# Kernel tuning notes

Hardware: AMD Instinct MI355X
Metric: run time of the kernel (lower is better)

## Reference

```python
import jax, jax.numpy as jnp
import numpy as np

D_MODEL = 1024
NUM_HEADS = 16
D_HEAD = D_MODEL // NUM_HEADS
THETA = 10000.0


def setup_inputs() -> dict:
    key = jax.random.key(0)
    ks = jax.random.split(key, 5)
    B, S = 2, 2048
    std = np.sqrt(2.0 / (D_MODEL + D_MODEL))
    return {
        "x": jax.random.normal(ks[0], (B, S, D_MODEL), dtype=jnp.float32),
        "token_positions": jnp.arange(S, dtype=jnp.int32),
        "wq": jax.random.normal(ks[1], (D_MODEL, D_MODEL), dtype=jnp.float32) * std,
        "wk": jax.random.normal(ks[2], (D_MODEL, D_MODEL), dtype=jnp.float32) * std,
        "wv": jax.random.normal(ks[3], (D_MODEL, D_MODEL), dtype=jnp.float32) * std,
        "wo": jax.random.normal(ks[4], (D_MODEL, D_MODEL), dtype=jnp.float32) * std,
    }


def _rope(x, token_positions):
    # x: [B, H, S, D_HEAD]; token_positions: [S]
    freq_idx = jnp.arange(0, D_HEAD, 2, dtype=jnp.float32)
    inv_freq = THETA ** (-freq_idx / D_HEAD)                      # [D_HEAD/2]
    angles = token_positions.astype(jnp.float32)[:, None] * inv_freq  # [S, D_HEAD/2]
    cos = jnp.cos(angles)[None, None, :, :]
    sin = jnp.sin(angles)[None, None, :, :]
    x_even = x[..., 0::2]
    x_odd = x[..., 1::2]
    rot_even = x_even * cos - x_odd * sin
    rot_odd = x_even * sin + x_odd * cos
    # interleave pairs back: [..., pairs, 2] -> [..., D_HEAD]
    return jnp.stack((rot_even, rot_odd), axis=-1).reshape(x.shape)


def reference(x, token_positions, wq, wk, wv, wo):
    B, S, _ = x.shape
    def proj(w):
        y = jnp.einsum('bsi,oi->bso', x, w)
        return y.reshape(B, S, NUM_HEADS, D_HEAD).transpose(0, 2, 1, 3)  # [B,H,S,Dh]
    q = _rope(proj(wq), token_positions)
    k = _rope(proj(wk), token_positions)
    v = proj(wv)
    scores = jnp.einsum('bhqd,bhkd->bhqk', q, k) / jnp.sqrt(jnp.float32(D_HEAD))
    causal = jnp.tril(jnp.ones((S, S), dtype=bool))
    scores = jnp.where(causal, scores, -jnp.inf)
    probs = jax.nn.softmax(scores, axis=-1)
    attn = jnp.einsum('bhqk,bhkd->bhqd', probs, v)
    attn = attn.transpose(0, 2, 1, 3).reshape(B, S, D_MODEL)
    return jnp.einsum('bsi,oi->bso', attn, wo)
```

## Files before the change

kernel.cpp:

```cpp
#include <hip/hip_runtime.h>
#include <math.h>

#define D_MODEL 1024
#define NUM_HEADS 16
#define D_HEAD 64
#define SEQ 2048
#define BATCH 2

typedef __attribute__((ext_vector_type(8))) short short8;
typedef __attribute__((ext_vector_type(4))) short short4v;
typedef __attribute__((ext_vector_type(4))) float float4v;

__device__ __forceinline__ short f2bf(float f) {
    unsigned u = __float_as_uint(f);
    u += 0x7FFFu + ((u >> 16) & 1u);
    return (short)(u >> 16);
}

__global__ __launch_bounds__(256) void cvt_bf16_kernel(
    const float* __restrict__ x,  const float* __restrict__ wq,
    const float* __restrict__ wk, const float* __restrict__ wv,
    const float* __restrict__ wo, const int* __restrict__ pos,
    short* __restrict__ xb,  short* __restrict__ wqb,
    short* __restrict__ wkb, short* __restrict__ wvb,
    short* __restrict__ wob,
    float* __restrict__ costab, float* __restrict__ sintab)
{
    const int a = blockIdx.y;
    if (a == 5) {
        const int idx = blockIdx.x * 256 + threadIdx.x;
        if (idx < SEQ * 32) {
            const int s = idx >> 5, fi = idx & 31;
            const float p = (float)pos[s];
            const float inv_freq = exp2f((float)fi * -0.4152410118609203f);
            float sn, cs;
            sincosf(p * inv_freq, &sn, &cs);
            costab[idx] = cs;
            sintab[idx] = sn;
        }
        return;
    }
    const float* src = (a == 0) ? x : (a == 1) ? wq : (a == 2) ? wk : (a == 3) ? wv : wo;
    short* dst = (a == 0) ? xb : (a == 1) ? wqb : (a == 2) ? wkb : (a == 3) ? wvb : wob;
    const int n = (a == 0) ? (BATCH * SEQ * D_MODEL) : (D_MODEL * D_MODEL);
    const int i = (blockIdx.x * 256 + threadIdx.x) * 8;
    if (i >= n) return;
    const float4 v0 = *(const float4*)(src + i);
    const float4 v1 = *(const float4*)(src + i + 4);
    short8 r;
    r[0] = f2bf(v0.x); r[1] = f2bf(v0.y); r[2] = f2bf(v0.z); r[3] = f2bf(v0.w);
    r[4] = f2bf(v1.x); r[5] = f2bf(v1.y); r[6] = f2bf(v1.z); r[7] = f2bf(v1.w);
    *(short8*)(dst + i) = r;
}

__device__ __forceinline__ void gemm_core_db(
    const short* __restrict__ a, const short* __restrict__ b,
    short* smem, int m0, int n0, float4v acc[4][4])
{
    const int tid = threadIdx.x;
    const int lane = tid & 63;
    const int l15 = lane & 15, quad = lane >> 4;
    const int wave = tid >> 6;
    const int mw = (wave & 1) * 64, nw = (wave >> 1) * 64;
    const int srow = tid >> 2;
    const int scol = (tid & 3) * 8;

    const short* ag = a + (size_t)(m0 + srow) * D_MODEL + scol;
    const short* bg = b + (size_t)(n0 + srow) * D_MODEL + scol;

    short* bufA[2] = { smem,        smem + 8192 };
    short* bufB[2] = { smem + 4096, smem + 12288 };

    short8 ga0 = *(const short8*)(ag);
    short8 ga1 = *(const short8*)(ag + (size_t)64 * D_MODEL);
    short8 gb0 = *(const short8*)(bg);
    short8 gb1 = *(const short8*)(bg + (size_t)64 * D_MODEL);
    *(short8*)&bufA[0][srow * 32 + scol]        = ga0;
    *(short8*)&bufA[0][(64 + srow) * 32 + scol] = ga1;
    *(short8*)&bufB[0][srow * 32 + scol]        = gb0;
    *(short8*)&bufB[0][(64 + srow) * 32 + scol] = gb1;
    ga0 = *(const short8*)(ag + 32);
    ga1 = *(const short8*)(ag + 32 + (size_t)64 * D_MODEL);
    gb0 = *(const short8*)(bg + 32);
    gb1 = *(const short8*)(bg + 32 + (size_t)64 * D_MODEL);

    for (int k = 0; k < 32; k++) {
        __syncthreads();
        if (k + 1 < 32) {
            short* bA = bufA[(k + 1) & 1];
            short* bB = bufB[(k + 1) & 1];
            *(short8*)&bA[srow * 32 + scol]        = ga0;
            *(short8*)&bA[(64 + srow) * 32 + scol] = ga1;
            *(short8*)&bB[srow * 32 + scol]        = gb0;
            *(short8*)&bB[(64 + srow) * 32 + scol] = gb1;
        }
        if (k + 2 < 32) {
            const int off = (k + 2) * 32;
            ga0 = *(const short8*)(ag + off);
            ga1 = *(const short8*)(ag + off + (size_t)64 * D_MODEL);
            gb0 = *(const short8*)(bg + off);
            gb1 = *(const short8*)(bg + off + (size_t)64 * D_MODEL);
        }
        const short* lA = bufA[k & 1];
        const short* lB = bufB[k & 1];
        short8 af[4], bf[4];
        #pragma unroll
        for (int i = 0; i < 4; i++)
            af[i] = *(const short8*)&lA[(mw + i * 16 + l15) * 32 + quad * 8];
        #pragma unroll
        for (int i = 0; i < 4; i++)
            bf[i] = *(const short8*)&lB[(nw + i * 16 + l15) * 32 + quad * 8];
        #pragma unroll
        for (int mi = 0; mi < 4; mi++)
            #pragma unroll
            for (int ni = 0; ni < 4; ni++)
                acc[mi][ni] = __builtin_amdgcn_mfma_f32_16x16x32_bf16(
                    af[mi], bf[ni], acc[mi][ni], 0, 0, 0);
    }
}

__global__ __launch_bounds__(256) void qkv_mfma_kernel(
    const short* __restrict__ xb, const short* __restrict__ wqb,
    const short* __restrict__ wkb, const short* __restrict__ wvb,
    const float* __restrict__ costab, const float* __restrict__ sintab,
    short* __restrict__ Qb, short* __restrict__ Kb, short* __restrict__ Vt)
{
    __shared__ __align__(16) short smem[128 * 136];

    const int z = blockIdx.x >> 8;
    const int bid = blockIdx.x & 255;
    const int m0 = (bid & 31) * 128;
    const int n0 = (bid >> 5) * 128;
    const short* w = (z == 0) ? wqb : (z == 1) ? wkb : wvb;

    float4v acc[4][4];
    #pragma unroll
    for (int i = 0; i < 4; i++)
        #pragma unroll
        for (int j = 0; j < 4; j++)
            acc[i][j] = (float4v){0.f, 0.f, 0.f, 0.f};

    gemm_core_db(xb, w, smem, m0, n0, acc);

    const int tid = threadIdx.x;
    const int lane = tid & 63;
    const int l15 = lane & 15, quad = lane >> 4;
    const int wave = tid >> 6;
    const int mw = (wave & 1) * 64, nw = (wave >> 1) * 64;
    const int s_base = m0 & (SEQ - 1);
    const int bb = m0 >> 11;

    __syncthreads();

    if (z == 2) {
        #pragma unroll
        for (int ni = 0; ni < 4; ni++) {
            #pragma unroll
            for (int mi = 0; mi < 4; mi++) {
                #pragma unroll
                for (int r = 0; r < 4; r++)
                    smem[(nw + ni * 16 + l15) * 136 + mw + mi * 16 + quad * 4 + r] =
                        f2bf(acc[mi][ni][r]);
            }
        }
        __syncthreads();
        #pragma unroll
        for (int it = 0; it < 8; it++) {
            const int nloc = it * 16 + (tid >> 4);
            const int mloc = (tid & 15) * 8;
            const short8 val = *(const short8*)&smem[nloc * 136 + mloc];
            const int n = n0 + nloc;
            const int h = n >> 6, d = n & 63;
            *(short8*)(Vt + ((size_t)(bb * NUM_HEADS + h) * D_HEAD + d) * SEQ +
                       s_base + mloc) = val;
        }
    } else {
        short* dst = (z == 0) ? Qb : Kb;
        const float qs = (z == 0) ? 0.125f : 1.0f;
        #pragma unroll
        for (int ni = 0; ni < 4; ni++) {
            const int n = n0 + nw + ni * 16 + l15;
            const int d = n & 63;
            const int fi = d >> 1;
            #pragma unroll
            for (int mi = 0; mi < 4; mi++) {
                #pragma unroll
                for (int r = 0; r < 4; r++) {
                    const int mloc = mw + mi * 16 + quad * 4 + r;
                    const int ti = ((s_base + mloc) << 5) + fi;
                    const float cs = costab[ti];
                    const float sn = sintab[ti];
                    const float val = acc[mi][ni][r];
                    const float partner = __shfl_xor(val, 1, 64);
                    const float res = (l15 & 1) ? fmaf(partner, sn, val * cs)
                                                : fmaf(val, cs, -partner * sn);
                    smem[mloc * 136 + nw + ni * 16 + l15] = f2bf(res * qs);
                }
            }
        }
        __syncthreads();
        #pragma unroll
        for (int it = 0; it < 8; it++) {
            const int ri = it * 32 + (tid >> 3);
            const int mloc = ri & 127;
            const int hh = ri >> 7;
            const int nloc = hh * 64 + (tid & 7) * 8;
            const short8 val = *(const short8*)&smem[mloc * 136 + nloc];
            const int n = n0 + nloc;
            const int h = n >> 6, d = n & 63;
            *(short8*)(dst + ((size_t)(bb * NUM_HEADS + h) * SEQ + s_base + mloc) *
                       D_HEAD + d) = val;
        }
    }
}

__global__ __launch_bounds__(256) void attn_mfma_kernel(
    const short* __restrict__ Qb, const short* __restrict__ Kb,
    const short* __restrict__ Vt, short* __restrict__ Ab)
{
    __shared__ __align__(16) short lK[64 * 72];
    __shared__ __align__(16) short lV[64 * 72];
    __shared__ __align__(16) short lP[4][16 * 72];

    const int tid = threadIdx.x;
    const int lane = tid & 63;
    const int wave = tid >> 6;
    const int l15 = lane & 15;
    const int quad = lane >> 4;

    const int bh = blockIdx.x & (BATCH * NUM_HEADS - 1);
    const int qt = (SEQ / 64 - 1) - (blockIdx.x >> 5);
    const int q0w = qt * 64 + wave * 16;
    const int qcmp = q0w + l15;

    const short* Kg = Kb + (size_t)bh * SEQ * D_HEAD;
    const short* Vg = Vt + (size_t)bh * D_HEAD * SEQ;

    const short* Qrow = Qb + ((size_t)bh * SEQ + q0w + l15) * D_HEAD;
    const short8 qf0 = *(const short8*)(Qrow + quad * 8);
    const short8 qf1 = *(const short8*)(Qrow + 32 + quad * 8);

    float4v o0 = {0.f, 0.f, 0.f, 0.f}, o1 = o0, o2 = o0, o3 = o0;
    float lp = 0.f;

    const int nt = qt + 1;
    const int srow = tid >> 2;
    const int sch = (tid & 3) * 8;

    short8 k0 = *(const short8*)(Kg + (size_t)srow * D_HEAD + sch);
    short8 k1 = *(const short8*)(Kg + (size_t)srow * D_HEAD + sch + 32);
    short8 v0 = *(const short8*)(Vg + (size_t)srow * SEQ + sch);
    short8 v1 = *(const short8*)(Vg + (size_t)srow * SEQ + sch + 32);

    for (int t = 0; t < nt; t++) {
        const int kt0 = t * 64;
        __syncthreads();
        *(short8*)&lK[srow * 72 + sch]      = k0;
        *(short8*)&lK[srow * 72 + sch + 32] = k1;
        *(short8*)&lV[srow * 72 + sch]      = v0;
        *(short8*)&lV[srow * 72 + sch + 32] = v1;
        __syncthreads();
        if (t + 1 < nt) {
            k0 = *(const short8*)(Kg + (size_t)(kt0 + 64 + srow) * D_HEAD + sch);
            k1 = *(const short8*)(Kg + (size_t)(kt0 + 64 + srow) * D_HEAD + sch + 32);
            v0 = *(const short8*)(Vg + (size_t)srow * SEQ + kt0 + 64 + sch);
            v1 = *(const short8*)(Vg + (size_t)srow * SEQ + kt0 + 64 + sch + 32);
        }

        short* Pw = lP[wave];
        #pragma unroll
        for (int g = 0; g < 4; g++) {
            float4v s = {0.f, 0.f, 0.f, 0.f};
            const short8 ka = *(const short8*)&lK[(g * 16 + l15) * 72 + quad * 8];
            s = __builtin_amdgcn_mfma_f32_16x16x32_bf16(ka, qf0, s, 0, 0, 0);
            const short8 kb = *(const short8*)&lK[(g * 16 + l15) * 72 + 32 + quad * 8];
            s = __builtin_amdgcn_mfma_f32_16x16x32_bf16(kb, qf1, s, 0, 0, 0);

            const int kbase = kt0 + g * 16 + quad * 4;
            short4v pk;
            #pragma unroll
            for (int r = 0; r < 4; r++) {
                const float e = (kbase + r <= qcmp) ? __expf(s[r]) : 0.f;
                lp += e;
                pk[r] = f2bf(e);
            }
            *(short4v*)&Pw[l15 * 72 + g * 16 + quad * 4] = pk;
        }

        const short8 pa0 = *(const short8*)&lP[wave][l15 * 72 + quad * 8];
        const short8 pa1 = *(const short8*)&lP[wave][l15 * 72 + 32 + quad * 8];

        {
            const short8 va = *(const short8*)&lV[(0 * 16 + l15) * 72 + quad * 8];
            const short8 vb = *(const short8*)&lV[(0 * 16 + l15) * 72 + 32 + quad * 8];
            o0 = __builtin_amdgcn_mfma_f32_16x16x32_bf16(pa0, va, o0, 0, 0, 0);
            o0 = __builtin_amdgcn_mfma_f32_16x16x32_bf16(pa1, vb, o0, 0, 0, 0);
        }
        {
            const short8 va = *(const short8*)&lV[(1 * 16 + l15) * 72 + quad * 8];
            const short8 vb = *(const short8*)&lV[(1 * 16 + l15) * 72 + 32 + quad * 8];
            o1 = __builtin_amdgcn_mfma_f32_16x16x32_bf16(pa0, va, o1, 0, 0, 0);
            o1 = __builtin_amdgcn_mfma_f32_16x16x32_bf16(pa1, vb, o1, 0, 0, 0);
        }
        {
            const short8 va = *(const short8*)&lV[(2 * 16 + l15) * 72 + quad * 8];
            const short8 vb = *(const short8*)&lV[(2 * 16 + l15) * 72 + 32 + quad * 8];
            o2 = __builtin_amdgcn_mfma_f32_16x16x32_bf16(pa0, va, o2, 0, 0, 0);
            o2 = __builtin_amdgcn_mfma_f32_16x16x32_bf16(pa1, vb, o2, 0, 0, 0);
        }
        {
            const short8 va = *(const short8*)&lV[(3 * 16 + l15) * 72 + quad * 8];
            const short8 vb = *(const short8*)&lV[(3 * 16 + l15) * 72 + 32 + quad * 8];
            o3 = __builtin_amdgcn_mfma_f32_16x16x32_bf16(pa0, va, o3, 0, 0, 0);
            o3 = __builtin_amdgcn_mfma_f32_16x16x32_bf16(pa1, vb, o3, 0, 0, 0);
        }
    }

    lp += __shfl_xor(lp, 16, 64);
    lp += __shfl_xor(lp, 32, 64);

    const int b = bh >> 4, h = bh & 15;
    short* Ap = Ab + ((size_t)(b * SEQ) + q0w + quad * 4) * D_MODEL + h * D_HEAD;
    #pragma unroll
    for (int r = 0; r < 4; r++) {
        const float inv = 1.0f / __shfl(lp, quad * 4 + r, 64);
        Ap[(size_t)r * D_MODEL + l15]      = f2bf(o0[r] * inv);
        Ap[(size_t)r * D_MODEL + 16 + l15] = f2bf(o1[r] * inv);
        Ap[(size_t)r * D_MODEL + 32 + l15] = f2bf(o2[r] * inv);
        Ap[(size_t)r * D_MODEL + 48 + l15] = f2bf(o3[r] * inv);
    }
}

__global__ __launch_bounds__(256) void out_mfma_kernel(
    const short* __restrict__ Ab, const short* __restrict__ wob,
    float* __restrict__ out)
{
    __shared__ __align__(16) short smem[2 * 8192];

    const int bid = blockIdx.x;
    const int m0 = (bid & 31) * 128;
    const int n0 = (bid >> 5) * 128;

    float4v acc[4][4];
    #pragma unroll
    for (int i = 0; i < 4; i++)
        #pragma unroll
        for (int j = 0; j < 4; j++)
            acc[i][j] = (float4v){0.f, 0.f, 0.f, 0.f};

    gemm_core_db(Ab, wob, smem, m0, n0, acc);

    const int tid = threadIdx.x;
    const int lane = tid & 63;
    const int l15 = lane & 15, quad = lane >> 4;
    const int wave = tid >> 6;
    const int mw = (wave & 1) * 64, nw = (wave >> 1) * 64;

    #pragma unroll
    for (int mi = 0; mi < 4; mi++) {
        #pragma unroll
        for (int r = 0; r < 4; r++) {
            const int m = m0 + mw + mi * 16 + quad * 4 + r;
            float* op = out + (size_t)m * D_MODEL + n0 + nw + l15;
            #pragma unroll
            for (int ni = 0; ni < 4; ni++)
                op[ni * 16] = acc[mi][ni][r];
        }
    }
}

extern "C" void kernel_launch(void* const* d_in, const int* in_sizes, int n_in,
                              void* d_out, int out_size, void* d_ws, size_t ws_size,
                              hipStream_t stream)
{
    const float* x  = (const float*)d_in[0];
    const int*  pos = (const int*)d_in[1];
    const float* wq = (const float*)d_in[2];
    const float* wk = (const float*)d_in[3];
    const float* wv = (const float*)d_in[4];
    const float* wo = (const float*)d_in[5];
    float* out = (float*)d_out;

    const size_t nx = (size_t)BATCH * SEQ * D_MODEL;
    const size_t nw = (size_t)D_MODEL * D_MODEL;
    short* xb  = (short*)d_ws;
    short* wqb = xb + nx;
    short* wkb = wqb + nw;
    short* wvb = wkb + nw;
    short* wob = wvb + nw;
    short* Qb  = wob + nw;
    short* Kb  = Qb + nx;
    short* Vt  = Kb + nx;
    short* Ab  = Vt + nx;
    float* costab = (float*)(Ab + nx);
    float* sintab = costab + SEQ * 32;

    dim3 blk(256);
    cvt_bf16_kernel<<<dim3(2048, 6), blk, 0, stream>>>(x, wq, wk, wv, wo, pos,
                                                       xb, wqb, wkb, wvb, wob,
                                                       costab, sintab);
    qkv_mfma_kernel<<<dim3(768), blk, 0, stream>>>(xb, wqb, wkb, wvb,
                                                   costab, sintab, Qb, Kb, Vt);
    attn_mfma_kernel<<<dim3(BATCH * NUM_HEADS * (SEQ / 64)), blk, 0, stream>>>(Qb, Kb, Vt, Ab);
    out_mfma_kernel<<<dim3(256), blk, 0, stream>>>(Ab, wob, out);
}
```

Baseline: 187.8 us.

## Load GEMM tiles directly into LDS with global_load_lds, single-buffered

Replaces the register-staged, double-buffered GEMM tile loads with direct global-to-LDS loads (global_load_lds, 16 bytes per lane), and shrinks the out-projection shared-memory buffer to one stage. This removes the VGPR round-trip and the separate LDS store instructions and may improve occupancy through lower LDS and register use. In exchange it drops the prefetch overlap: each k-step now issues its loads and waits on a barrier before computing, so load latency is exposed unless other resident blocks hide it.

```diff
diff --git a/kernel.cpp b/kernel.cpp
--- a/kernel.cpp
+++ b/kernel.cpp
@@ -16,6 +16,11 @@
     u += 0x7FFFu + ((u >> 16) & 1u);
     return (short)(u >> 16);
 }
+
+#define GLOAD_LDS16(g, l)                                                     \
+    __builtin_amdgcn_global_load_lds(                                         \
+        (const __attribute__((address_space(1))) unsigned int*)(g),           \
+        (__attribute__((address_space(3))) unsigned int*)(l), 16, 0, 0)
 
 __global__ __launch_bounds__(256) void cvt_bf16_kernel(
     const float* __restrict__ x,  const float* __restrict__ wq,
@@ -53,9 +58,9 @@
     *(short8*)(dst + i) = r;
 }
 
-__device__ __forceinline__ void gemm_core_db(
+__device__ __forceinline__ void gemm_core_lds(
     const short* __restrict__ a, const short* __restrict__ b,
-    short* smem, int m0, int n0, float4v acc[4][4])
+    short* lA, short* lB, int m0, int n0, float4v acc[4][4])
 {
     const int tid = threadIdx.x;
     const int lane = tid & 63;
@@ -67,42 +72,17 @@
 
     const short* ag = a + (size_t)(m0 + srow) * D_MODEL + scol;
     const short* bg = b + (size_t)(n0 + srow) * D_MODEL + scol;
-
-    short* bufA[2] = { smem,        smem + 8192 };
-    short* bufB[2] = { smem + 4096, smem + 12288 };
-
-    short8 ga0 = *(const short8*)(ag);
-    short8 ga1 = *(const short8*)(ag + (size_t)64 * D_MODEL);
-    short8 gb0 = *(const short8*)(bg);
-    short8 gb1 = *(const short8*)(bg + (size_t)64 * D_MODEL);
-    *(short8*)&bufA[0][srow * 32 + scol]        = ga0;
-    *(short8*)&bufA[0][(64 + srow) * 32 + scol] = ga1;
-    *(short8*)&bufB[0][srow * 32 + scol]        = gb0;
-    *(short8*)&bufB[0][(64 + srow) * 32 + scol] = gb1;
-    ga0 = *(const short8*)(ag + 32);
-    ga1 = *(const short8*)(ag + 32 + (size_t)64 * D_MODEL);
-    gb0 = *(const short8*)(bg + 32);
-    gb1 = *(const short8*)(bg + 32 + (size_t)64 * D_MODEL);
-
-    for (int k = 0; k < 32; k++) {
-        __syncthreads();
-        if (k + 1 < 32) {
-            short* bA = bufA[(k + 1) & 1];
-            short* bB = bufB[(k + 1) & 1];
-            *(short8*)&bA[srow * 32 + scol]        = ga0;
-            *(short8*)&bA[(64 + srow) * 32 + scol] = ga1;
-            *(short8*)&bB[srow * 32 + scol]        = gb0;
-            *(short8*)&bB[(64 + srow) * 32 + scol] = gb1;
-        }
-        if (k + 2 < 32) {
-            const int off = (k + 2) * 32;
-            ga0 = *(const short8*)(ag + off);
-            ga1 = *(const short8*)(ag + off + (size_t)64 * D_MODEL);
-            gb0 = *(const short8*)(bg + off);
-            gb1 = *(const short8*)(bg + off + (size_t)64 * D_MODEL);
-        }
-        const short* lA = bufA[k & 1];
-        const short* lB = bufB[k & 1];
+    short* lAd = lA + tid * 8;
+    short* lBd = lB + tid * 8;
+
+    for (int k0 = 0; k0 < D_MODEL; k0 += 32) {
+        __syncthreads();
+        GLOAD_LDS16(ag + k0, lAd);
+        GLOAD_LDS16(ag + k0 + (size_t)64 * D_MODEL, lAd + 2048);
+        GLOAD_LDS16(bg + k0, lBd);
+        GLOAD_LDS16(bg + k0 + (size_t)64 * D_MODEL, lBd + 2048);
+        __syncthreads();
+
         short8 af[4], bf[4];
         #pragma unroll
         for (int i = 0; i < 4; i++)
@@ -140,7 +120,7 @@
         for (int j = 0; j < 4; j++)
             acc[i][j] = (float4v){0.f, 0.f, 0.f, 0.f};
 
-    gemm_core_db(xb, w, smem, m0, n0, acc);
+    gemm_core_lds(xb, w, smem, smem + 4096, m0, n0, acc);
 
     const int tid = threadIdx.x;
     const int lane = tid & 63;
@@ -335,7 +315,7 @@
     const short* __restrict__ Ab, const short* __restrict__ wob,
     float* __restrict__ out)
 {
-    __shared__ __align__(16) short smem[2 * 8192];
+    __shared__ __align__(16) short smem[8192];
 
     const int bid = blockIdx.x;
     const int m0 = (bid & 31) * 128;
@@ -348,7 +328,7 @@
         for (int j = 0; j < 4; j++)
             acc[i][j] = (float4v){0.f, 0.f, 0.f, 0.f};
 
-    gemm_core_db(Ab, wob, smem, m0, n0, acc);
+    gemm_core_lds(Ab, wob, smem, smem + 4096, m0, n0, acc);
 
     const int tid = threadIdx.x;
     const int lane = tid & 63;
```

Measured after the change: 214.1 us. 14.0% more time.

## Process two 64-row query tiles per attention block to reuse K/V loads

Applied to the files above, without the earlier changes.

Each attention workgroup now handles 128 query rows, with every wave owning two 16-row query groups (A and B), so each K/V tile staged in LDS is reused by twice as many queries. The grid is halved and the upper group's extra causal tile runs only the B path through a per-wave activity check. This cuts global K/V traffic and barrier count per query. The cost is more registers and LDS per block, fewer blocks for the causal load-balance, and some wave divergence on the last tile.

```diff
diff --git a/kernel.cpp b/kernel.cpp
--- a/kernel.cpp
+++ b/kernel.cpp
@@ -220,7 +220,8 @@
 {
     __shared__ __align__(16) short lK[64 * 72];
     __shared__ __align__(16) short lV[64 * 72];
-    __shared__ __align__(16) short lP[4][16 * 72];
+    __shared__ __align__(16) short lPA[4][16 * 72];
+    __shared__ __align__(16) short lPB[4][16 * 72];
 
     const int tid = threadIdx.x;
     const int lane = tid & 63;
@@ -229,21 +230,28 @@
     const int quad = lane >> 4;
 
     const int bh = blockIdx.x & (BATCH * NUM_HEADS - 1);
-    const int qt = (SEQ / 64 - 1) - (blockIdx.x >> 5);
-    const int q0w = qt * 64 + wave * 16;
-    const int qcmp = q0w + l15;
+    const int qt = (SEQ / 128 - 1) - (blockIdx.x >> 5);
+    const int q0b = qt * 128;
+    const int qA = q0b + wave * 16;
+    const int qB = qA + 64;
+    const int qcA = qA + l15;
+    const int qcB = qB + l15;
 
     const short* Kg = Kb + (size_t)bh * SEQ * D_HEAD;
     const short* Vg = Vt + (size_t)bh * D_HEAD * SEQ;
 
-    const short* Qrow = Qb + ((size_t)bh * SEQ + q0w + l15) * D_HEAD;
-    const short8 qf0 = *(const short8*)(Qrow + quad * 8);
-    const short8 qf1 = *(const short8*)(Qrow + 32 + quad * 8);
-
-    float4v o0 = {0.f, 0.f, 0.f, 0.f}, o1 = o0, o2 = o0, o3 = o0;
-    float lp = 0.f;
-
-    const int nt = qt + 1;
+    const short* QrowA = Qb + ((size_t)bh * SEQ + qA + l15) * D_HEAD;
+    const short8 qa0 = *(const short8*)(QrowA + quad * 8);
+    const short8 qa1 = *(const short8*)(QrowA + 32 + quad * 8);
+    const short* QrowB = Qb + ((size_t)bh * SEQ + qB + l15) * D_HEAD;
+    const short8 qb0 = *(const short8*)(QrowB + quad * 8);
+    const short8 qb1 = *(const short8*)(QrowB + 32 + quad * 8);
+
+    float4v oA0 = {0.f,0.f,0.f,0.f}, oA1 = oA0, oA2 = oA0, oA3 = oA0;
+    float4v oB0 = oA0, oB1 = oA0, oB2 = oA0, oB3 = oA0;
+    float lpA = 0.f, lpB = 0.f;
+
+    const int nt = (qt + 1) * 2;
     const int srow = tid >> 2;
     const int sch = (tid & 3) * 8;
 
@@ -267,67 +275,90 @@
             v1 = *(const short8*)(Vg + (size_t)srow * SEQ + kt0 + 64 + sch + 32);
         }
 
-        short* Pw = lP[wave];
+        const bool actA = (kt0 <= qA + 15);
+
         #pragma unroll
         for (int g = 0; g < 4; g++) {
-            float4v s = {0.f, 0.f, 0.f, 0.f};
             const short8 ka = *(const short8*)&lK[(g * 16 + l15) * 72 + quad * 8];
-            s = __builtin_amdgcn_mfma_f32_16x16x32_bf16(ka, qf0, s, 0, 0, 0);
             const short8 kb = *(const short8*)&lK[(g * 16 + l15) * 72 + 32 + quad * 8];
-            s = __builtin_amdgcn_mfma_f32_16x16x32_bf16(kb, qf1, s, 0, 0, 0);
-
             const int kbase = kt0 + g * 16 + quad * 4;
-            short4v pk;
-            #pragma unroll
-            for (int r = 0; r < 4; r++) {
-                const float e = (kbase + r <= qcmp) ? __expf(s[r]) : 0.f;
-                lp += e;
-                pk[r] = f2bf(e);
-            }
-            *(short4v*)&Pw[l15 * 72 + g * 16 + quad * 4] = pk;
-        }
-
-        const short8 pa0 = *(const short8*)&lP[wave][l15 * 72 + quad * 8];
-        const short8 pa1 = *(const short8*)&lP[wave][l15 * 72 + 32 + quad * 8];
-
-        {
-            const short8 va = *(const short8*)&lV[(0 * 16 + l15) * 72 + quad * 8];
-            const short8 vb = *(const short8*)&lV[(0 * 16 + l15) * 72 + 32 + quad * 8];
-            o0 = __builtin_amdgcn_mfma_f32_16x16x32_bf16(pa0, va, o0, 0, 0, 0);
-            o0 = __builtin_amdgcn_mfma_f32_16x16x32_bf16(pa1, vb, o0, 0, 0, 0);
-        }
-        {
-            const short8 va = *(const short8*)&lV[(1 * 16 + l15) * 72 + quad * 8];
-            const short8 vb = *(const short8*)&lV[(1 * 16 + l15) * 72 + 32 + quad * 8];
-            o1 = __builtin_amdgcn_mfma_f32_16x16x32_bf16(pa0, va, o1, 0, 0, 0);
-            o1 = __builtin_amdgcn_mfma_f32_16x16x32_bf16(pa1, vb, o1, 0, 0, 0);
-        }
-        {
-            const short8 va = *(const short8*)&lV[(2 * 16 + l15) * 72 + quad * 8];
-            const short8 vb = *(const short8*)&lV[(2 * 16 + l15) * 72 + 32 + quad * 8];
-            o2 = __builtin_amdgcn_mfma_f32_16x16x32_bf16(pa0, va, o2, 0, 0, 0);
-            o2 = __builtin_amdgcn_mfma_f32_16x16x32_bf16(pa1, vb, o2, 0, 0, 0);
-        }
-        {
-            const short8 va = *(const short8*)&lV[(3 * 16 + l15) * 72 + quad * 8];
-            const short8 vb = *(const short8*)&lV[(3 * 16 + l15) * 72 + 32 + quad * 8];
-            o3 = __builtin_amdgcn_mfma_f32_16x16x32_bf16(pa0, va, o3, 0, 0, 0);
-            o3 = __builtin_amdgcn_mfma_f32_16x16x32_bf16(pa1, vb, o3, 0, 0, 0);
-        }
-    }
-
-    lp += __shfl_xor(lp, 16, 64);
-    lp += __shfl_xor(lp, 32, 64);
+
+            if (actA) {
+                float4v s = {0.f, 0.f, 0.f, 0.f};
+                s = __builtin_amdgcn_mfma_f32_16x16x32_bf16(ka, qa0, s, 0, 0, 0);
+                s = __builtin_amdgcn_mfma_f32_16x16x32_bf16(kb, qa1, s, 0, 0, 0);
+                short4v pk;
+                #pragma unroll
+                for (int r = 0; r < 4; r++) {
+                    const float e = (kbase + r <= qcA) ? __expf(s[r]) : 0.f;
+                    lpA += e;
+                    pk[r] = f2bf(e);
+                }
+                *(short4v*)&lPA[wave][l15 * 72 + g * 16 + quad * 4] = pk;
+            }
+            {
+                float4v s = {0.f, 0.f, 0.f, 0.f};
+                s = __builtin_amdgcn_mfma_f32_16x16x32_bf16(ka, qb0, s, 0, 0, 0);
+                s = __builtin_amdgcn_mfma_f32_16x16x32_bf16(kb, qb1, s, 0, 0, 0);
+                short4v pk;
+                #pragma unroll
+                for (int r = 0; r < 4; r++) {
+                    const float e = (kbase + r <= qcB) ? __expf(s[r]) : 0.f;
+                    lpB += e;
+                    pk[r] = f2bf(e);
+                }
+                *(short4v*)&lPB[wave][l15 * 72 + g * 16 + quad * 4] = pk;
+            }
+        }
+
+        const short8 pb0 = *(const short8*)&lPB[wave][l15 * 72 + quad * 8];
+        const short8 pb1 = *(const short8*)&lPB[wave][l15 * 72 + 32 + quad * 8];
+        if (actA) {
+            const short8 pa0 = *(const short8*)&lPA[wave][l15 * 72 + quad * 8];
+            const short8 pa1 = *(const short8*)&lPA[wave][l15 * 72 + 32 + quad * 8];
+            #pragma unroll
+            for (int gg = 0; gg < 4; gg++) {
+                const short8 va = *(const short8*)&lV[(gg * 16 + l15) * 72 + quad * 8];
+                const short8 vb = *(const short8*)&lV[(gg * 16 + l15) * 72 + 32 + quad * 8];
+                float4v* oA = (gg == 0) ? &oA0 : (gg == 1) ? &oA1 : (gg == 2) ? &oA2 : &oA3;
+                float4v* oB = (gg == 0) ? &oB0 : (gg == 1) ? &oB1 : (gg == 2) ? &oB2 : &oB3;
+                *oA = __builtin_amdgcn_mfma_f32_16x16x32_bf16(pa0, va, *oA, 0, 0, 0);
+                *oA = __builtin_amdgcn_mfma_f32_16x16x32_bf16(pa1, vb, *oA, 0, 0, 0);
+                *oB = __builtin_amdgcn_mfma_f32_16x16x32_bf16(pb0, va, *oB, 0, 0, 0);
+                *oB = __builtin_amdgcn_mfma_f32_16x16x32_bf16(pb1, vb, *oB, 0, 0, 0);
+            }
+        } else {
+            #pragma unroll
+            for (int gg = 0; gg < 4; gg++) {
+                const short8 va = *(const short8*)&lV[(gg * 16 + l15) * 72 + quad * 8];
+                const short8 vb = *(const short8*)&lV[(gg * 16 + l15) * 72 + 32 + quad * 8];
+                float4v* oB = (gg == 0) ? &oB0 : (gg == 1) ? &oB1 : (gg == 2) ? &oB2 : &oB3;
+                *oB = __builtin_amdgcn_mfma_f32_16x16x32_bf16(pb0, va, *oB, 0, 0, 0);
+                *oB = __builtin_amdgcn_mfma_f32_16x16x32_bf16(pb1, vb, *oB, 0, 0, 0);
+            }
+        }
+    }
+
+    lpA += __shfl_xor(lpA, 16, 64);
+    lpA += __shfl_xor(lpA, 32, 64);
+    lpB += __shfl_xor(lpB, 16, 64);
+    lpB += __shfl_xor(lpB, 32, 64);
 
     const int b = bh >> 4, h = bh & 15;
-    short* Ap = Ab + ((size_t)(b * SEQ) + q0w + quad * 4) * D_MODEL + h * D_HEAD;
+    short* ApA = Ab + ((size_t)(b * SEQ) + qA + quad * 4) * D_MODEL + h * D_HEAD;
+    short* ApB = Ab + ((size_t)(b * SEQ) + qB + quad * 4) * D_MODEL + h * D_HEAD;
     #pragma unroll
     for (int r = 0; r < 4; r++) {
-        const float inv = 1.0f / __shfl(lp, quad * 4 + r, 64);
-        Ap[(size_t)r * D_MODEL + l15]      = f2bf(o0[r] * inv);
-        Ap[(size_t)r * D_MODEL + 16 + l15] = f2bf(o1[r] * inv);
-        Ap[(size_t)r * D_MODEL + 32 + l15] = f2bf(o2[r] * inv);
-        Ap[(size_t)r * D_MODEL + 48 + l15] = f2bf(o3[r] * inv);
+        const float invA = 1.0f / __shfl(lpA, quad * 4 + r, 64);
+        ApA[(size_t)r * D_MODEL + l15]      = f2bf(oA0[r] * invA);
+        ApA[(size_t)r * D_MODEL + 16 + l15] = f2bf(oA1[r] * invA);
+        ApA[(size_t)r * D_MODEL + 32 + l15] = f2bf(oA2[r] * invA);
+        ApA[(size_t)r * D_MODEL + 48 + l15] = f2bf(oA3[r] * invA);
+        const float invB = 1.0f / __shfl(lpB, quad * 4 + r, 64);
+        ApB[(size_t)r * D_MODEL + l15]      = f2bf(oB0[r] * invB);
+        ApB[(size_t)r * D_MODEL + 16 + l15] = f2bf(oB1[r] * invB);
+        ApB[(size_t)r * D_MODEL + 32 + l15] = f2bf(oB2[r] * invB);
+        ApB[(size_t)r * D_MODEL + 48 + l15] = f2bf(oB3[r] * invB);
     }
 }
 
@@ -401,6 +432,6 @@
                                                        costab, sintab);
     qkv_mfma_kernel<<<dim3(768), blk, 0, stream>>>(xb, wqb, wkb, wvb,
                                                    costab, sintab, Qb, Kb, Vt);
-    attn_mfma_kernel<<<dim3(BATCH * NUM_HEADS * (SEQ / 64)), blk, 0, stream>>>(Qb, Kb, Vt, Ab);
+    attn_mfma_kernel<<<dim3(BATCH * NUM_HEADS * (SEQ / 128)), blk, 0, stream>>>(Qb, Kb, Vt, Ab);
     out_mfma_kernel<<<dim3(256), blk, 0, stream>>>(Ab, wob, out);
 }
```

After: 198.5 us. +5.7%, slower.
